# Performance work log

Measured on AMD Instinct MI355X. Metric: run time of the kernel, lower is better.

The kernel has to match this reference:

```python
import jax, jax.numpy as jnp
import numpy as np

N = 200_000
E = 6_400_000
EPS = 1e-12


def l2_normalize(x):
    # F.normalize(x, p=2, dim=1): x / max(||x||_2, eps)
    n = jnp.linalg.norm(x, axis=1, keepdims=True)
    return x / jnp.maximum(n, EPS)


def gcn_conv(x, W, b, src, dst, n):
    """PyG GCNConv: add self-loops, symmetric normalization D^-1/2 A D^-1/2,
    linear transform (no bias) on nodes, scatter-add to targets, then + bias."""
    loop = jnp.arange(n)
    s = jnp.concatenate([src, loop])  # sources (messages gathered here)
    d = jnp.concatenate([dst, loop])  # targets (aggregation here)
    deg = jax.ops.segment_sum(jnp.ones(s.shape[0], dtype=x.dtype), d, num_segments=n)
    dinv = jnp.where(deg > 0, jax.lax.rsqrt(deg), 0.0)
    norm = dinv[s] * dinv[d]  # [E+N]
    h = x @ W  # [N, out]
    out = jax.ops.segment_sum(norm[:, None] * h[s], d, num_segments=n)
    return out + b


def setup_inputs() -> dict:
    key = jax.random.key(0)
    ks = jax.random.split(key, 10)
    x = jax.random.normal(ks[0], (N, 3), dtype=jnp.float32)
    edge_index = jax.random.randint(ks[1], (2, E), 0, N, dtype=jnp.int64)

    def glorot(k, shape):
        lim = float(np.sqrt(6.0 / (shape[0] + shape[1])))
        return jax.random.uniform(k, shape, jnp.float32, -lim, lim)

    return {
        "x": x,
        "edge_index": edge_index,
        "W1": glorot(ks[2], (3, 6)),   "b1": jnp.zeros((6,), jnp.float32),
        "W2": glorot(ks[3], (6, 12)),  "b2": jnp.zeros((12,), jnp.float32),
        "W3": glorot(ks[4], (12, 24)), "b3": jnp.zeros((24,), jnp.float32),
        "Wc": glorot(ks[5], (24, 13)), "bc": jnp.zeros((13,), jnp.float32),
    }


def reference(x, edge_index, W1, b1, W2, b2, W3, b3, Wc, bc):
    src, dst = edge_index[0], edge_index[1]
    n = x.shape[0]
    h = jnp.tanh(gcn_conv(x, W1, b1, src, dst, n))
    h = jnp.tanh(l2_normalize(gcn_conv(h, W2, b2, src, dst, n)))
    h = l2_normalize(gcn_conv(h, W3, b3, src, dst, n))
    h = h @ Wc + bc
    return l2_normalize(h)
```

## Files before the change

### kernel.cpp

```cpp
#include <hip/hip_runtime.h>
#include <math.h>


static constexpr int NN = 200000;
static constexpr int NE = 6400000;
static constexpr int BK = 256;

static constexpr int SUBW  = 512;
static constexpr int NBA   = (NN + SUBW - 1) / SUBW;
static constexpr int CAP   = 24;
static constexpr int FLUSH = 16;
static constexpr int CAPB  = 18400;
static constexpr int BKP   = 512;
static constexpr int EPT   = 4;
static constexpr int CHUNK = BKP * EPT;
static constexpr int GPART = 1024;
static constexpr int SRCSH = 13;
static constexpr int NSB   = (NN + (1 << SRCSH) - 1) >> SRCSH;

static constexpr int S     = 4;
static constexpr int LOGS  = 2;

__global__ void __launch_bounds__(BKP) k_part(const int* __restrict__ srcI,
                                              const int* __restrict__ dstI,
                                              unsigned* __restrict__ stg,
                                              int* __restrict__ gtail,
                                              int* __restrict__ work, int e) {
  __shared__ unsigned bin[NBA][CAP];
  __shared__ int bcnt[NBA];
  __shared__ int curc;
  for (int t = threadIdx.x; t < NBA; t += BKP) bcnt[t] = 0;
  __syncthreads();
  int nchunks = (e + CHUNK - 1) / CHUNK;
  for (;;) {
    if (threadIdx.x == 0) curc = atomicAdd(work, 1);
    __syncthreads();
    int c = curc;
    if (c >= nchunks) break;
    int base_i = c * CHUNK;
    int dv[EPT], sv[EPT];
#pragma unroll
    for (int u = 0; u < EPT; ++u) {
      int i = base_i + u * BKP + (int)threadIdx.x;
      dv[u] = (i < e) ? __builtin_nontemporal_load(dstI + i) : -1;
      sv[u] = (i < e) ? __builtin_nontemporal_load(srcI + i) : 0;
    }
#pragma unroll
    for (int u = 0; u < EPT; ++u) {
      if (dv[u] >= 0) {
        int b = dv[u] >> 9;
        unsigned rec = ((unsigned)(dv[u] & (SUBW - 1)) << 18) | (unsigned)sv[u];
        int p = atomicAdd(&bcnt[b], 1);
        if (p < CAP) {
          bin[b][p] = rec;
        } else {
          int base = atomicAdd(&gtail[b], 1);
          stg[(size_t)b * CAPB + base] = rec;
        }
      }
    }
    __syncthreads();
    int b2 = threadIdx.x;
    if (b2 < NBA) {
      int c2 = bcnt[b2];
      if (c2 > CAP) c2 = CAP;
      if (c2 >= FLUSH) {
        int nfl = c2 & ~(FLUSH - 1);
        int base = atomicAdd(&gtail[b2], nfl);
        size_t o = (size_t)b2 * CAPB + base;
        for (int k = 0; k < nfl; k += 4)
          *(uint4*)(stg + o + k) = *(const uint4*)&bin[b2][k];
        int r = c2 - nfl;
        for (int k = 0; k < r; ++k) bin[b2][k] = bin[b2][nfl + k];
        bcnt[b2] = r;
      }
    }
    __syncthreads();
  }
  int b2 = threadIdx.x;
  if (b2 < NBA) {
    int c2 = bcnt[b2];
    if (c2 > CAP) c2 = CAP;
    if (c2 > 0) {
      int base = atomicAdd(&gtail[b2], c2);
      size_t o = (size_t)b2 * CAPB + base;
      for (int k = 0; k < c2; ++k) stg[o + k] = bin[b2][k];
    }
  }
}

__global__ void __launch_bounds__(BK) k_build(const unsigned* __restrict__ stg,
                                              const int* __restrict__ gtail,
                                              int* __restrict__ rowptr,
                                              int* __restrict__ adj,
                                              int* __restrict__ b8,
                                              int* __restrict__ b13,
                                              int* __restrict__ b17) {
  __shared__ unsigned hist2[SUBW * NSB];
  __shared__ int htot[SUBW];
  __shared__ int s0[SUBW], s1[SUBW];
  __shared__ int red[BK];
  int b = blockIdx.x;
  {
    int ssum = 0;
    for (int t = threadIdx.x; t < b; t += BK) ssum += gtail[t];
    red[threadIdx.x] = ssum;
    __syncthreads();
    for (int o = BK / 2; o > 0; o >>= 1) {
      if (threadIdx.x < o) red[threadIdx.x] += red[threadIdx.x + o];
      __syncthreads();
    }
  }
  int base = red[0];
  int m = gtail[b]; if (m > CAPB) m = CAPB;
  size_t off = (size_t)b * CAPB;
  if (b == NBA - 1 && threadIdx.x == 0) rowptr[NN] = base + m;
  for (int t = threadIdx.x; t < SUBW * NSB; t += BK) hist2[t] = 0;
  __syncthreads();
  for (int k = threadIdx.x; k < m; k += BK) {
    unsigned rec = stg[off + k];
    int dl = rec >> 18;
    int sb = (int)((rec & 0x3FFFFu) >> SRCSH);
    atomicAdd(&hist2[dl * NSB + sb], 1u);
  }
  __syncthreads();
  for (int dl = threadIdx.x; dl < SUBW; dl += BK) {
    unsigned run = 0;
    for (int sb = 0; sb < NSB; ++sb) {
      unsigned c = hist2[dl * NSB + sb];
      hist2[dl * NSB + sb] = run;
      run += c;
    }
    htot[dl] = (int)run;
    s0[dl] = (int)run;
  }
  __syncthreads();
  int* a = s0; int* bb = s1;
  for (int o2 = 1; o2 < SUBW; o2 <<= 1) {
    for (int t = threadIdx.x; t < SUBW; t += BK) bb[t] = a[t] + ((t >= o2) ? a[t - o2] : 0);
    __syncthreads();
    int* tmp = a; a = bb; bb = tmp;
  }
  for (int t = threadIdx.x; t < SUBW; t += BK) {
    int node = b * SUBW + t;
    int ex = a[t] - htot[t];
    if (node < NN) {
      rowptr[node] = base + ex;
      b8[node]  = base + ex + (int)hist2[t * NSB + 8];
      b13[node] = base + ex + (int)hist2[t * NSB + 13];
      b17[node] = base + ex + (int)hist2[t * NSB + 17];
    }
    bb[t] = ex;
  }
  __syncthreads();
  for (int k = threadIdx.x; k < m; k += BK) {
    unsigned rec = stg[off + k];
    int dl = rec >> 18;
    unsigned src = rec & 0x3FFFFu;
    int sb = (int)(src >> SRCSH);
    int p = bb[dl] + (int)atomicAdd(&hist2[dl * NSB + sb], 1u);
    adj[base + p] = (int)src;
  }
}

__global__ void k_zero(int* __restrict__ p, int n) {
  int i = blockIdx.x * blockDim.x + threadIdx.x;
  if (i < n) p[i] = 0;
}

__global__ void k_prep(const float* __restrict__ x, const int* __restrict__ rowptr,
                       float* __restrict__ dinv, float* __restrict__ p1, int n) {
  int i = blockIdx.x * blockDim.x + threadIdx.x;
  if (i >= n) return;
  float di = rsqrtf(1.0f + (float)(rowptr[i + 1] - rowptr[i]));
  dinv[i] = di;
  float3 v;
  v.x = di * x[3 * (size_t)i];
  v.y = di * x[3 * (size_t)i + 1];
  v.z = di * x[3 * (size_t)i + 2];
  *(float3*)(p1 + 3 * (size_t)i) = v;
}

template <int RW> struct RowT;
template <> struct RowT<3> {
  using T = float3;
  static __device__ inline T ld(const float* __restrict__ p) { return *(const float3*)p; }
  static __device__ inline void add(float* __restrict__ a, const T& v) {
    a[0] += v.x; a[1] += v.y; a[2] += v.z;
  }
  static __device__ inline void st(float* __restrict__ p, const float* __restrict__ a) {
    *(float3*)p = make_float3(a[0], a[1], a[2]);
  }
};
template <> struct RowT<6> {
  struct T { float2 a, b, c; };
  static __device__ inline T ld(const float* __restrict__ p) {
    T t; t.a = *(const float2*)p; t.b = *(const float2*)(p + 2); t.c = *(const float2*)(p + 4);
    return t;
  }
  static __device__ inline void add(float* __restrict__ a, const T& v) {
    a[0] += v.a.x; a[1] += v.a.y; a[2] += v.b.x; a[3] += v.b.y; a[4] += v.c.x; a[5] += v.c.y;
  }
  static __device__ inline void st(float* __restrict__ p, const float* __restrict__ a) {
    *(float2*)(p)     = make_float2(a[0], a[1]);
    *(float2*)(p + 2) = make_float2(a[2], a[3]);
    *(float2*)(p + 4) = make_float2(a[4], a[5]);
  }
};
template <> struct RowT<12> {
  struct T { float4 a, b, c; };
  static __device__ inline T ld(const float* __restrict__ p) {
    T t; t.a = *(const float4*)p; t.b = *(const float4*)(p + 4); t.c = *(const float4*)(p + 8);
    return t;
  }
  static __device__ inline void add(float* __restrict__ a, const T& v) {
    a[0] += v.a.x; a[1] += v.a.y; a[2] += v.a.z; a[3] += v.a.w;
    a[4] += v.b.x; a[5] += v.b.y; a[6] += v.b.z; a[7] += v.b.w;
    a[8] += v.c.x; a[9] += v.c.y; a[10] += v.c.z; a[11] += v.c.w;
  }
  static __device__ inline void st(float* __restrict__ p, const float* __restrict__ a) {
    *(float4*)(p)     = make_float4(a[0], a[1], a[2], a[3]);
    *(float4*)(p + 4) = make_float4(a[4], a[5], a[6], a[7]);
    *(float4*)(p + 8) = make_float4(a[8], a[9], a[10], a[11]);
  }
};

template <int RW, int UN>
__device__ inline void gather_p(const int* __restrict__ adj, int st, int en,
                                const float* __restrict__ pin, float* __restrict__ acc,
                                int slot) {
  using RT = RowT<RW>;
  using T = typename RT::T;
  int k = st + slot;
  if (k + (UN - 1) * S < en) {
    int a[UN];
#pragma unroll
    for (int u = 0; u < UN; ++u) a[u] = adj[k + u * S];
    for (;;) {
      int kn = k + UN * S;
      bool more = (kn + (UN - 1) * S < en);
      int b[UN];
#pragma unroll
      for (int u = 0; u < UN; ++u) b[u] = 0;
      if (more) {
#pragma unroll
        for (int u = 0; u < UN; ++u) b[u] = adj[kn + u * S];
      }
      T v[UN];
#pragma unroll
      for (int u = 0; u < UN; ++u) v[u] = RT::ld(pin + (size_t)a[u] * RW);
#pragma unroll
      for (int u = 0; u < UN; ++u) RT::add(acc, v[u]);
      k = kn;
      if (!more) break;
#pragma unroll
      for (int u = 0; u < UN; ++u) a[u] = b[u];
    }
  }
  for (; k < en; k += S) {
    T v = RT::ld(pin + (size_t)adj[k] * RW);
    RT::add(acc, v);
  }
}

template <int FIN>
__device__ inline void group_reduce(float* __restrict__ acc) {
#pragma unroll
  for (int j = 0; j < FIN; ++j) {
    acc[j] += __shfl_xor(acc[j], 1);
    acc[j] += __shfl_xor(acc[j], 2);
  }
}

template <int RW, int FOUT, int MODE>
__global__ void __launch_bounds__(BK, 8) k_gather_fused(
    const int* __restrict__ adj, const int* __restrict__ rowptr,
    const float* __restrict__ pin, const float* __restrict__ W,
    const float* __restrict__ bias, const float* __restrict__ dinv,
    float* __restrict__ pout, int n) {
  __shared__ float sW[RW * FOUT];
  __shared__ float sb[FOUT];
  for (int t = threadIdx.x; t < RW * FOUT; t += BK) sW[t] = W[t];
  if (threadIdx.x < FOUT) sb[threadIdx.x] = bias[threadIdx.x];
  __syncthreads();
  int g = blockIdx.x * blockDim.x + threadIdx.x;
  int i = g >> LOGS;
  int slot = g & (S - 1);
  if (i >= n) return;
  float acc[RW] = {};
  if (slot == 0) {
    typename RowT<RW>::T v = RowT<RW>::ld(pin + (size_t)i * RW);
    RowT<RW>::add(acc, v);
  }
  gather_p<RW, 4>(adj, rowptr[i], rowptr[i + 1], pin, acc, slot);
  group_reduce<RW>(acc);
  float di = dinv[i];
  float h[FOUT];
  float ss = 0.f;
#pragma unroll
  for (int j = 0; j < FOUT; ++j) {
    float s = 0.f;
#pragma unroll
    for (int kk = 0; kk < RW; ++kk) s = fmaf(acc[kk], sW[kk * FOUT + j], s);
    float t = fmaf(di, s, sb[j]);
    h[j] = t;
    ss += t * t;
  }
  float o[FOUT];
  if (MODE == 0) {
#pragma unroll
    for (int j = 0; j < FOUT; ++j) o[j] = di * tanhf(h[j]);
  } else {
    float inv = 1.f / fmaxf(sqrtf(ss), 1e-12f);
#pragma unroll
    for (int j = 0; j < FOUT; ++j) o[j] = di * tanhf(h[j] * inv);
  }
  if (slot == 0) {
    float* po = pout + (size_t)i * FOUT;
    if (MODE == 0) {
      *(float2*)(po)     = make_float2(o[0], o[1]);
      *(float2*)(po + 2) = make_float2(o[2], o[3]);
      *(float2*)(po + 4) = make_float2(o[4], o[5]);
    } else {
      *(float4*)(po)     = make_float4(o[0], o[1], o[2], o[3]);
      *(float4*)(po + 4) = make_float4(o[4], o[5], o[6], o[7]);
      *(float4*)(po + 8) = make_float4(o[8], o[9], o[10], o[11]);
    }
  }
}

template <int RW, bool FIRST>
__global__ void __launch_bounds__(BK, 8) k_gphase(
    const int* __restrict__ adj, const int* __restrict__ stA,
    const int* __restrict__ enB, const float* __restrict__ pin,
    float* __restrict__ accb, int n) {
  int g = blockIdx.x * blockDim.x + threadIdx.x;
  int i = g >> LOGS;
  int slot = g & (S - 1);
  if (i >= n) return;
  float acc[RW] = {};
  if (slot == 0) {
    if (FIRST) {
      typename RowT<RW>::T v = RowT<RW>::ld(pin + (size_t)i * RW);
      RowT<RW>::add(acc, v);
    } else {
      typename RowT<RW>::T v = RowT<RW>::ld(accb + (size_t)i * RW);
      RowT<RW>::add(acc, v);
    }
  }
  gather_p<RW, 4>(adj, stA[i], enB[i], pin, acc, slot);
  group_reduce<RW>(acc);
  if (slot == 0) RowT<RW>::st(accb + (size_t)i * RW, acc);
}

template <int RW, int FOUT, int MODE>
__global__ void __launch_bounds__(BK, 6) k_gphase_last(
    const int* __restrict__ adj, const int* __restrict__ stA,
    const int* __restrict__ rowptr, const float* __restrict__ pin,
    const float* __restrict__ W, const float* __restrict__ bias,
    const float* __restrict__ Wc, const float* __restrict__ bc,
    const float* __restrict__ dinv, const float* __restrict__ accb,
    float* __restrict__ out, int n) {
  constexpr int FC = 13;
  __shared__ float sW[RW * FOUT];
  __shared__ float sb[FOUT];
  __shared__ float sWc[MODE == 2 ? FOUT * FC : 1];
  __shared__ float sbc[MODE == 2 ? FC : 1];
  for (int t = threadIdx.x; t < RW * FOUT; t += BK) sW[t] = W[t];
  if (threadIdx.x < FOUT) sb[threadIdx.x] = bias[threadIdx.x];
  if (MODE == 2) {
    for (int t = threadIdx.x; t < FOUT * FC; t += BK) sWc[t] = Wc[t];
    if (threadIdx.x < FC) sbc[threadIdx.x] = bc[threadIdx.x];
  }
  __syncthreads();
  int g = blockIdx.x * blockDim.x + threadIdx.x;
  int i = g >> LOGS;
  int slot = g & (S - 1);
  if (i >= n) return;
  float acc[RW] = {};
  if (slot == 0) {
    typename RowT<RW>::T v = RowT<RW>::ld(accb + (size_t)i * RW);
    RowT<RW>::add(acc, v);
  }
  gather_p<RW, 4>(adj, stA[i], rowptr[i + 1], pin, acc, slot);
  group_reduce<RW>(acc);
  float di = dinv[i];
  float h[FOUT];
  float ss = 0.f;
#pragma unroll
  for (int j = 0; j < FOUT; ++j) {
    float s = 0.f;
#pragma unroll
    for (int kk = 0; kk < RW; ++kk) s = fmaf(acc[kk], sW[kk * FOUT + j], s);
    float t = fmaf(di, s, sb[j]);
    h[j] = t;
    ss += t * t;
  }
  float inv = 1.f / fmaxf(sqrtf(ss), 1e-12f);
  if (MODE == 1) {
    float o[FOUT];
#pragma unroll
    for (int j = 0; j < FOUT; ++j) o[j] = di * tanhf(h[j] * inv);
    if (slot == 0) {
      float* po = out + (size_t)i * FOUT;
      *(float4*)(po)     = make_float4(o[0], o[1], o[2], o[3]);
      *(float4*)(po + 4) = make_float4(o[4], o[5], o[6], o[7]);
      *(float4*)(po + 8) = make_float4(o[8], o[9], o[10], o[11]);
    }
  } else {
    float v[FC];
    float ss2 = 0.f;
#pragma unroll
    for (int j = 0; j < FC; ++j) {
      float s = sbc[j];
#pragma unroll
      for (int kk = 0; kk < FOUT; ++kk) s = fmaf(h[kk] * inv, sWc[kk * FC + j], s);
      v[j] = s;
      ss2 += s * s;
    }
    float inv2 = 1.f / fmaxf(sqrtf(ss2), 1e-12f);
    if (slot == 0) {
#pragma unroll
      for (int j = 0; j < FC; ++j) out[(size_t)i * FC + j] = v[j] * inv2;
    }
  }
}

extern "C" void kernel_launch(void* const* d_in, const int* in_sizes, int n_in,
                              void* d_out, int out_size, void* d_ws, size_t ws_size,
                              hipStream_t stream) {
  const float* x  = (const float*)d_in[0];
  const int*   ei = (const int*)d_in[1];
  const float* W1 = (const float*)d_in[2];
  const float* b1 = (const float*)d_in[3];
  const float* W2 = (const float*)d_in[4];
  const float* b2 = (const float*)d_in[5];
  const float* W3 = (const float*)d_in[6];
  const float* b3 = (const float*)d_in[7];
  const float* Wc = (const float*)d_in[8];
  const float* bc = (const float*)d_in[9];
  float* out = (float*)d_out;

  const int n = NN;
  const int e = NE;
  const int* srcI = ei;
  const int* dstI = ei + e;

  float* ws = (float*)d_ws;
  float* dinv  = ws;
  int* rowptr  = (int*)(ws + n);
  int* gtail   = rowptr + n + 8;
  int* work    = gtail + 512;
  int* adj     = work + 16;
  int* b8      = adj + e;
  int* b13     = b8 + n;
  int* b17     = b13 + n;
  size_t roff = (size_t)n + (n + 8) + 512 + 16 + e + 3 * (size_t)n;
  roff = (roff + 15) & ~(size_t)15;
  float* R     = ws + roff;
  unsigned* stg = (unsigned*)R;
  float* p1   = R;
  float* p2   = R + (size_t)3 * n;
  float* p3   = R + (size_t)9 * n;
  float* accb = R + (size_t)21 * n;

  const int gn  = (n + BK - 1) / BK;
  const int gnS = (n * S + BK - 1) / BK;

  k_zero<<<3, BK, 0, stream>>>(gtail, 528);
  k_part<<<GPART, BKP, 0, stream>>>(srcI, dstI, stg, gtail, work, e);
  k_build<<<NBA, BK, 0, stream>>>(stg, gtail, rowptr, adj, b8, b13, b17);

  k_prep<<<gn, BK, 0, stream>>>(x, rowptr, dinv, p1, n);

  k_gather_fused<3, 6, 0><<<gnS, BK, 0, stream>>>(adj, rowptr, p1, W1, b1, dinv, p2, n);

  k_gphase<6, true><<<gnS, BK, 0, stream>>>(adj, rowptr, b13, p2, accb, n);
  k_gphase_last<6, 12, 1><<<gnS, BK, 0, stream>>>(adj, b13, rowptr, p2, W2, b2,
                                                  Wc, bc, dinv, accb, p3, n);

  k_gphase<12, true><<<gnS, BK, 0, stream>>>(adj, rowptr, b8, p3, accb, n);
  k_gphase<12, false><<<gnS, BK, 0, stream>>>(adj, b8, b17, p3, accb, n);
  k_gphase_last<12, 24, 2><<<gnS, BK, 0, stream>>>(adj, b17, rowptr, p3, W3, b3,
                                                   Wc, bc, dinv, accb, out, n);
}
```

Before: 463.3 us.

## Replace atomic shared-bin partitioning with count-scan-scatter radix partition

Replaces the dynamic work-stealing partition kernel, which used shared-memory bins flushed to global staging with global atomics, by a deterministic three-pass counting sort: per-block histograms of destination bins, a two-level prefix scan, then a scatter into compact offsets. This removes the global atomic tail counters, the per-block flush synchronisation and the fixed-capacity per-bin staging, and it drops the zeroing kernel. In exchange, dst is read twice, scattered single-word writes replace vectorised flushes, and there are three extra small kernel launches.

Result: no change. 457.5 us (-1.2%).

```diff
diff --git a/kernel.cpp b/kernel.cpp
--- a/kernel.cpp
+++ b/kernel.cpp
@@ -8,89 +8,118 @@
 
 static constexpr int SUBW  = 512;
 static constexpr int NBA   = (NN + SUBW - 1) / SUBW;
-static constexpr int CAP   = 24;
-static constexpr int FLUSH = 16;
-static constexpr int CAPB  = 18400;
-static constexpr int BKP   = 512;
-static constexpr int EPT   = 4;
-static constexpr int CHUNK = BKP * EPT;
-static constexpr int GPART = 1024;
+static constexpr int NBL   = 512;
+static constexpr int BKC   = 512;
+static constexpr int SEG   = (NE + NBL - 1) / NBL;
 static constexpr int SRCSH = 13;
 static constexpr int NSB   = (NN + (1 << SRCSH) - 1) >> SRCSH;
 
 static constexpr int S     = 4;
 static constexpr int LOGS  = 2;
 
-__global__ void __launch_bounds__(BKP) k_part(const int* __restrict__ srcI,
+__global__ void __launch_bounds__(BKC) k_count(const int* __restrict__ dstI,
+                                               int* __restrict__ hist, int e) {
+  __shared__ int cnt[NBA];
+  for (int t = threadIdx.x; t < NBA; t += BKC) cnt[t] = 0;
+  __syncthreads();
+  int blk = blockIdx.x;
+  int st = blk * SEG, en = st + SEG; if (en > e) en = e;
+  int i = st + (int)threadIdx.x;
+  for (; i + 3 * BKC < en; i += 4 * BKC) {
+    int d0 = __builtin_nontemporal_load(dstI + i);
+    int d1 = __builtin_nontemporal_load(dstI + i + BKC);
+    int d2 = __builtin_nontemporal_load(dstI + i + 2 * BKC);
+    int d3 = __builtin_nontemporal_load(dstI + i + 3 * BKC);
+    atomicAdd(&cnt[d0 >> 9], 1);
+    atomicAdd(&cnt[d1 >> 9], 1);
+    atomicAdd(&cnt[d2 >> 9], 1);
+    atomicAdd(&cnt[d3 >> 9], 1);
+  }
+  for (; i < en; i += BKC) {
+    int d = __builtin_nontemporal_load(dstI + i);
+    atomicAdd(&cnt[d >> 9], 1);
+  }
+  __syncthreads();
+  for (int t = threadIdx.x; t < NBA; t += BKC) hist[(size_t)t * NBL + blk] = cnt[t];
+}
+
+__global__ void __launch_bounds__(256) k_scanrow(int* __restrict__ hist,
+                                                 int* __restrict__ tot) {
+  __shared__ int s0[256], s1[256];
+  int b = blockIdx.x, t = threadIdx.x;
+  int* row = hist + (size_t)b * NBL;
+  int v0 = row[2 * t], v1 = row[2 * t + 1];
+  int s = v0 + v1;
+  s0[t] = s;
+  __syncthreads();
+  int* a = s0; int* bb = s1;
+  for (int o = 1; o < 256; o <<= 1) {
+    bb[t] = a[t] + ((t >= o) ? a[t - o] : 0);
+    __syncthreads();
+    int* tmp = a; a = bb; bb = tmp;
+  }
+  int ex = a[t] - s;
+  row[2 * t] = ex;
+  row[2 * t + 1] = ex + v0;
+  if (t == 255) tot[b] = a[t];
+}
+
+__global__ void k_scanbin(const int* __restrict__ tot, int* __restrict__ sbase) {
+  __shared__ int s0[512], s1[512];
+  int t = threadIdx.x;
+  int v = (t < NBA) ? tot[t] : 0;
+  s0[t] = v;
+  __syncthreads();
+  int* a = s0; int* b = s1;
+  for (int o = 1; o < 512; o <<= 1) {
+    b[t] = a[t] + ((t >= o) ? a[t - o] : 0);
+    __syncthreads();
+    int* tmp = a; a = b; b = tmp;
+  }
+  if (t < NBA) sbase[t] = a[t] - v;
+  if (t == NBA - 1) sbase[NBA] = a[t];
+}
+
+__global__ void __launch_bounds__(BKC) k_scat(const int* __restrict__ srcI,
                                               const int* __restrict__ dstI,
-                                              unsigned* __restrict__ stg,
-                                              int* __restrict__ gtail,
-                                              int* __restrict__ work, int e) {
-  __shared__ unsigned bin[NBA][CAP];
-  __shared__ int bcnt[NBA];
-  __shared__ int curc;
-  for (int t = threadIdx.x; t < NBA; t += BKP) bcnt[t] = 0;
-  __syncthreads();
-  int nchunks = (e + CHUNK - 1) / CHUNK;
-  for (;;) {
-    if (threadIdx.x == 0) curc = atomicAdd(work, 1);
-    __syncthreads();
-    int c = curc;
-    if (c >= nchunks) break;
-    int base_i = c * CHUNK;
-    int dv[EPT], sv[EPT];
-#pragma unroll
-    for (int u = 0; u < EPT; ++u) {
-      int i = base_i + u * BKP + (int)threadIdx.x;
-      dv[u] = (i < e) ? __builtin_nontemporal_load(dstI + i) : -1;
-      sv[u] = (i < e) ? __builtin_nontemporal_load(srcI + i) : 0;
-    }
-#pragma unroll
-    for (int u = 0; u < EPT; ++u) {
-      if (dv[u] >= 0) {
-        int b = dv[u] >> 9;
-        unsigned rec = ((unsigned)(dv[u] & (SUBW - 1)) << 18) | (unsigned)sv[u];
-        int p = atomicAdd(&bcnt[b], 1);
-        if (p < CAP) {
-          bin[b][p] = rec;
-        } else {
-          int base = atomicAdd(&gtail[b], 1);
-          stg[(size_t)b * CAPB + base] = rec;
-        }
-      }
-    }
-    __syncthreads();
-    int b2 = threadIdx.x;
-    if (b2 < NBA) {
-      int c2 = bcnt[b2];
-      if (c2 > CAP) c2 = CAP;
-      if (c2 >= FLUSH) {
-        int nfl = c2 & ~(FLUSH - 1);
-        int base = atomicAdd(&gtail[b2], nfl);
-        size_t o = (size_t)b2 * CAPB + base;
-        for (int k = 0; k < nfl; k += 4)
-          *(uint4*)(stg + o + k) = *(const uint4*)&bin[b2][k];
-        int r = c2 - nfl;
-        for (int k = 0; k < r; ++k) bin[b2][k] = bin[b2][nfl + k];
-        bcnt[b2] = r;
-      }
-    }
-    __syncthreads();
-  }
-  int b2 = threadIdx.x;
-  if (b2 < NBA) {
-    int c2 = bcnt[b2];
-    if (c2 > CAP) c2 = CAP;
-    if (c2 > 0) {
-      int base = atomicAdd(&gtail[b2], c2);
-      size_t o = (size_t)b2 * CAPB + base;
-      for (int k = 0; k < c2; ++k) stg[o + k] = bin[b2][k];
-    }
+                                              const int* __restrict__ hist,
+                                              const int* __restrict__ sbase,
+                                              unsigned* __restrict__ stg, int e) {
+  __shared__ int cur[NBA];
+  int blk = blockIdx.x;
+  for (int t = threadIdx.x; t < NBA; t += BKC)
+    cur[t] = sbase[t] + hist[(size_t)t * NBL + blk];
+  __syncthreads();
+  int st = blk * SEG, en = st + SEG; if (en > e) en = e;
+  int i = st + (int)threadIdx.x;
+  for (; i + 3 * BKC < en; i += 4 * BKC) {
+    int s0v = __builtin_nontemporal_load(srcI + i);
+    int d0 = __builtin_nontemporal_load(dstI + i);
+    int s1v = __builtin_nontemporal_load(srcI + i + BKC);
+    int d1 = __builtin_nontemporal_load(dstI + i + BKC);
+    int s2v = __builtin_nontemporal_load(srcI + i + 2 * BKC);
+    int d2 = __builtin_nontemporal_load(dstI + i + 2 * BKC);
+    int s3v = __builtin_nontemporal_load(srcI + i + 3 * BKC);
+    int d3 = __builtin_nontemporal_load(dstI + i + 3 * BKC);
+    int p0 = atomicAdd(&cur[d0 >> 9], 1);
+    int p1 = atomicAdd(&cur[d1 >> 9], 1);
+    int p2 = atomicAdd(&cur[d2 >> 9], 1);
+    int p3 = atomicAdd(&cur[d3 >> 9], 1);
+    stg[p0] = ((unsigned)(d0 & (SUBW - 1)) << 18) | (unsigned)s0v;
+    stg[p1] = ((unsigned)(d1 & (SUBW - 1)) << 18) | (unsigned)s1v;
+    stg[p2] = ((unsigned)(d2 & (SUBW - 1)) << 18) | (unsigned)s2v;
+    stg[p3] = ((unsigned)(d3 & (SUBW - 1)) << 18) | (unsigned)s3v;
+  }
+  for (; i < en; i += BKC) {
+    int sv = __builtin_nontemporal_load(srcI + i);
+    int d = __builtin_nontemporal_load(dstI + i);
+    int p = atomicAdd(&cur[d >> 9], 1);
+    stg[p] = ((unsigned)(d & (SUBW - 1)) << 18) | (unsigned)sv;
   }
 }
 
 __global__ void __launch_bounds__(BK) k_build(const unsigned* __restrict__ stg,
-                                              const int* __restrict__ gtail,
+                                              const int* __restrict__ sbase,
                                               int* __restrict__ rowptr,
                                               int* __restrict__ adj,
                                               int* __restrict__ b8,
@@ -99,21 +128,10 @@
   __shared__ unsigned hist2[SUBW * NSB];
   __shared__ int htot[SUBW];
   __shared__ int s0[SUBW], s1[SUBW];
-  __shared__ int red[BK];
   int b = blockIdx.x;
-  {
-    int ssum = 0;
-    for (int t = threadIdx.x; t < b; t += BK) ssum += gtail[t];
-    red[threadIdx.x] = ssum;
-    __syncthreads();
-    for (int o = BK / 2; o > 0; o >>= 1) {
-      if (threadIdx.x < o) red[threadIdx.x] += red[threadIdx.x + o];
-      __syncthreads();
-    }
-  }
-  int base = red[0];
-  int m = gtail[b]; if (m > CAPB) m = CAPB;
-  size_t off = (size_t)b * CAPB;
+  int base = sbase[b];
+  int m = sbase[b + 1] - base;
+  size_t off = (size_t)base;
   if (b == NBA - 1 && threadIdx.x == 0) rowptr[NN] = base + m;
   for (int t = threadIdx.x; t < SUBW * NSB; t += BK) hist2[t] = 0;
   __syncthreads();
@@ -161,11 +179,6 @@
     int p = bb[dl] + (int)atomicAdd(&hist2[dl * NSB + sb], 1u);
     adj[base + p] = (int)src;
   }
-}
-
-__global__ void k_zero(int* __restrict__ p, int n) {
-  int i = blockIdx.x * blockDim.x + threadIdx.x;
-  if (i < n) p[i] = 0;
 }
 
 __global__ void k_prep(const float* __restrict__ x, const int* __restrict__ rowptr,
@@ -449,13 +462,14 @@
   float* ws = (float*)d_ws;
   float* dinv  = ws;
   int* rowptr  = (int*)(ws + n);
-  int* gtail   = rowptr + n + 8;
-  int* work    = gtail + 512;
-  int* adj     = work + 16;
+  int* sbase   = rowptr + n + 8;
+  int* tot     = sbase + 512;
+  int* hist    = tot + 512;
+  int* adj     = hist + NBA * NBL;
   int* b8      = adj + e;
   int* b13     = b8 + n;
   int* b17     = b13 + n;
-  size_t roff = (size_t)n + (n + 8) + 512 + 16 + e + 3 * (size_t)n;
+  size_t roff = (size_t)n + (n + 8) + 512 + 512 + (size_t)NBA * NBL + e + 3 * (size_t)n;
   roff = (roff + 15) & ~(size_t)15;
   float* R     = ws + roff;
   unsigned* stg = (unsigned*)R;
@@ -467,9 +481,11 @@
   const int gn  = (n + BK - 1) / BK;
   const int gnS = (n * S + BK - 1) / BK;
 
-  k_zero<<<3, BK, 0, stream>>>(gtail, 528);
-  k_part<<<GPART, BKP, 0, stream>>>(srcI, dstI, stg, gtail, work, e);
-  k_build<<<NBA, BK, 0, stream>>>(stg, gtail, rowptr, adj, b8, b13, b17);
+  k_count<<<NBL, BKC, 0, stream>>>(dstI, hist, e);
+  k_scanrow<<<NBA, 256, 0, stream>>>(hist, tot);
+  k_scanbin<<<1, 512, 0, stream>>>(tot, sbase);
+  k_scat<<<NBL, BKC, 0, stream>>>(srcI, dstI, hist, sbase, stg, e);
+  k_build<<<NBA, BK, 0, stream>>>(stg, sbase, rowptr, adj, b8, b13, b17);
 
   k_prep<<<gn, BK, 0, stream>>>(x, rowptr, dinv, p1, n);
 
```
